# Optimization experiments

Hardware: AMD Instinct MI355X
Metric: run time of the kernel (lower is better)

Reference implementation:

```python
import jax, jax.numpy as jnp
import numpy as np
from math import sqrt

EMBED = 768
HEADS = 12
EPS = 1e-12  # torch F.normalize eps


def setup_inputs() -> dict:
    key = jax.random.key(0)
    ks = jax.random.split(key, 9)
    B, N, E = 8, 4096, EMBED
    s = 1.0 / np.sqrt(E)
    x = jax.random.normal(ks[0], (B, N, E), dtype=jnp.float32)
    Wq = jax.random.normal(ks[1], (E, E), dtype=jnp.float32) * s
    bq = jnp.zeros((E,), dtype=jnp.float32)
    Wk = jax.random.normal(ks[2], (E, E), dtype=jnp.float32) * s
    bk = jnp.zeros((E,), dtype=jnp.float32)
    Wv = jax.random.normal(ks[3], (E, E), dtype=jnp.float32) * s
    bv = jnp.zeros((E,), dtype=jnp.float32)
    Wo = jax.random.normal(ks[4], (E, E), dtype=jnp.float32) * s
    bo = jnp.zeros((E,), dtype=jnp.float32)
    return {"x": x, "Wq": Wq, "bq": bq, "Wk": Wk, "bk": bk,
            "Wv": Wv, "bv": bv, "Wo": Wo, "bo": bo}


def _l2norm_tokens(t):
    # F.normalize(p=2, dim=1): normalize over the token (n) axis
    nrm = jnp.sqrt(jnp.sum(t * t, axis=1, keepdims=True))
    return t / jnp.maximum(nrm, EPS)


def reference(x, Wq, bq, Wk, bk, Wv, bv, Wo, bo):
    B, N, E = x.shape
    h = HEADS
    e = E // h
    q = (x @ Wq + bq).reshape(B, N, h, e)
    k = (x @ Wk + bk).reshape(B, N, h, e)
    v = (x @ Wv + bv).reshape(B, N, h, e)
    q = _l2norm_tokens(q)
    k = _l2norm_tokens(k)
    # cross-covariance attention over channel dim: [b, e, h, e]
    energy = jnp.einsum('bnhe,bnhq->behq', q, k)
    attn = jax.nn.softmax(energy, axis=-1) / sqrt(E)
    out = jnp.einsum('behq,bnhe->bnhq', attn, v)  # [b, n, h, e]
    out = out.reshape(B, N, E)
    return out @ Wo + bo
```

## Files before the change

kernel.cpp:

```cpp
#include <hip/hip_runtime.h>
#include <hip/hip_bf16.h>

typedef short bf16x8 __attribute__((ext_vector_type(8)));
typedef unsigned short u16x8 __attribute__((ext_vector_type(8)));
typedef float f32x4 __attribute__((ext_vector_type(4)));
using bf16 = __hip_bfloat16;

#define EMB 768
#define NHEAD 12
#define BATCH 8
#define NTOK 4096
#define BNTOK 32768

__device__ __forceinline__ float b2f(unsigned short u) {
    union { unsigned int i; float f; } x; x.i = ((unsigned int)u) << 16; return x.f;
}
__device__ __forceinline__ unsigned short f2bu(float f) {
    bf16 h = __float2bfloat16(f);
    return *reinterpret_cast<unsigned short*>(&h);
}

__device__ __forceinline__ void gload_lds16(const void* g, void* l) {
    __builtin_amdgcn_global_load_lds(
        (const __attribute__((address_space(1))) unsigned int*)g,
        (__attribute__((address_space(3))) unsigned int*)l,
        16, 0, 0);
}

__global__ __launch_bounds__(256) void cast_x_kernel(const float* __restrict__ x,
                                                     bf16* __restrict__ xb, int n8) {
    int i = blockIdx.x * blockDim.x + threadIdx.x;
    if (i >= n8) return;
    const float4* xv = (const float4*)x;
    float4 a = xv[i * 2], b = xv[i * 2 + 1];
    u16x8 o;
    o[0] = f2bu(a.x); o[1] = f2bu(a.y); o[2] = f2bu(a.z); o[3] = f2bu(a.w);
    o[4] = f2bu(b.x); o[5] = f2bu(b.y); o[6] = f2bu(b.z); o[7] = f2bu(b.w);
    ((u16x8*)xb)[i] = o;
}

__global__ __launch_bounds__(256) void prep_w_kernel(
    const float* __restrict__ Wq, const float* __restrict__ Wk,
    const float* __restrict__ Wv, const float* __restrict__ Wo,
    const float* __restrict__ bq, const float* __restrict__ bk, const float* __restrict__ bv,
    bf16* __restrict__ WqkvT, bf16* __restrict__ WoT, float* __restrict__ bqkv) {
    const int NQKV = 2304 * 768, NO = 768 * 768;
    int i = blockIdx.x * blockDim.x + threadIdx.x;
    if (i < NQKV) {
        int nrow = i / 768, k = i % 768;
        const float* W = (nrow < 768) ? Wq : (nrow < 1536 ? Wk : Wv);
        int c = nrow % 768;
        WqkvT[i] = __float2bfloat16(W[k * 768 + c]);
    } else if (i < NQKV + NO) {
        int j = i - NQKV; int nrow = j / 768, k = j % 768;
        WoT[j] = __float2bfloat16(Wo[k * 768 + nrow]);
    } else if (i < NQKV + NO + 2304) {
        int j = i - NQKV - NO;
        bqkv[j] = (j < 768) ? bq[j] : (j < 1536 ? bk[j - 768] : bv[j - 1536]);
    }
}

template <int MODE>
__global__ __launch_bounds__(256) void gemm_bt(
    const bf16* __restrict__ A, const bf16* __restrict__ BT,
    int M, int N, int K,
    bf16* __restrict__ Q, bf16* __restrict__ Kb, bf16* __restrict__ V,
    const float* __restrict__ bias,
    float* __restrict__ Cout, const float* __restrict__ bo) {
    __shared__ bf16 As[128 * 32];
    __shared__ bf16 Bs[128 * 32];
    const int tid = threadIdx.x;
    const int lane = tid & 63, wid = tid >> 6;
    const int wm = wid >> 1, wn = wid & 1;
    const int m0 = blockIdx.y * 128, n0 = blockIdx.x * 128;

    f32x4 acc[4][4] = {};
    const int nk = K >> 5;
    const int r0 = tid >> 2, k8 = (tid & 3) << 3;
    const int lrow = lane & 15, lk = lane >> 4;

    for (int kt = 0; kt < nk; ++kt) {
        const bf16* ga0 = A + (size_t)(m0 + r0) * K + kt * 32 + k8;
        const bf16* gb0 = BT + (size_t)(n0 + r0) * K + kt * 32 + k8;
        char* la0 = (char*)As + (wid * 64) * 16;
        char* la1 = (char*)As + (256 + wid * 64) * 16;
        char* lb0 = (char*)Bs + (wid * 64) * 16;
        char* lb1 = (char*)Bs + (256 + wid * 64) * 16;
        gload_lds16(ga0, la0);
        gload_lds16(ga0 + (size_t)64 * K, la1);
        gload_lds16(gb0, lb0);
        gload_lds16(gb0 + (size_t)64 * K, lb1);
        __syncthreads();
        const bf16x8* Av = (const bf16x8*)As;
        const bf16x8* Bv = (const bf16x8*)Bs;
        bf16x8 a[4], b[4];
#pragma unroll
        for (int i = 0; i < 4; ++i) a[i] = Av[(wm * 64 + i * 16 + lrow) * 4 + lk];
#pragma unroll
        for (int i = 0; i < 4; ++i) b[i] = Bv[(wn * 64 + i * 16 + lrow) * 4 + lk];
#pragma unroll
        for (int mi = 0; mi < 4; ++mi)
#pragma unroll
            for (int ni = 0; ni < 4; ++ni)
                acc[mi][ni] = __builtin_amdgcn_mfma_f32_16x16x32_bf16(a[mi], b[ni], acc[mi][ni], 0, 0, 0);
        __syncthreads();
    }

    const int lq = lane >> 4;
    if (MODE == 0) {
        const int which = n0 / 768;
        bf16* O = (which == 0) ? Q : (which == 1 ? Kb : V);
#pragma unroll
        for (int mi = 0; mi < 4; ++mi)
#pragma unroll
            for (int ni = 0; ni < 4; ++ni) {
                int gcol = n0 + wn * 64 + ni * 16 + lrow;
                int col = gcol - which * 768;
                float bia = bias[gcol];
                size_t rbase = (size_t)(m0 + wm * 64 + mi * 16 + lq * 4);
#pragma unroll
                for (int r = 0; r < 4; ++r)
                    O[(rbase + r) * 768 + col] = __float2bfloat16(acc[mi][ni][r] + bia);
            }
    } else {
#pragma unroll
        for (int mi = 0; mi < 4; ++mi)
#pragma unroll
            for (int ni = 0; ni < 4; ++ni) {
                int col = n0 + wn * 64 + ni * 16 + lrow;
                float bia = bo[col];
                size_t rbase = (size_t)(m0 + wm * 64 + mi * 16 + lq * 4);
#pragma unroll
                for (int r = 0; r < 4; ++r)
                    Cout[(rbase + r) * 768 + col] = acc[mi][ni][r] + bia;
            }
    }
}

__global__ __launch_bounds__(256) void sumsq_kernel(
    const bf16* __restrict__ Qb, const bf16* __restrict__ Kb,
    float* __restrict__ ssq, float* __restrict__ ssk) {
    int rc = blockIdx.x, ct = blockIdx.y, b = blockIdx.z;
    int col = ct * 256 + threadIdx.x;
    size_t base = ((size_t)b * NTOK + rc * 256) * 768 + col;
    float sq = 0.f, sk = 0.f;
    for (int i = 0; i < 256; ++i) {
        float q = b2f(*(const unsigned short*)&Qb[base + (size_t)i * 768]);
        float k = b2f(*(const unsigned short*)&Kb[base + (size_t)i * 768]);
        sq += q * q; sk += k * k;
    }
    atomicAdd(&ssq[b * 768 + col], sq);
    atomicAdd(&ssk[b * 768 + col], sk);
}

__global__ __launch_bounds__(256) void gram_kernel(
    const bf16* __restrict__ Qb, const bf16* __restrict__ Kb, float* __restrict__ G) {
    int bh = blockIdx.x >> 2, ch = blockIdx.x & 3;
    int b = bh / NHEAD, h = bh % NHEAD;
    const int t0 = ch * 1024;
    __shared__ float Qs[32][64];
    __shared__ float Ks[32][64];
    int tid = threadIdx.x;
    int e0 = (tid >> 4) << 2, j0 = (tid & 15) << 2;
    float acc[4][4] = {};
    const size_t base = ((size_t)b * NTOK) * 768 + h * 64;
    int lt = tid >> 3, lc = (tid & 7) << 3;
    for (int it = 0; it < 32; ++it) {
        int tok = t0 + it * 32;
        u16x8 qv = *(const u16x8*)(Qb + base + (size_t)(tok + lt) * 768 + lc);
        u16x8 kv = *(const u16x8*)(Kb + base + (size_t)(tok + lt) * 768 + lc);
        __syncthreads();
#pragma unroll
        for (int j = 0; j < 8; ++j) { Qs[lt][lc + j] = b2f(qv[j]); Ks[lt][lc + j] = b2f(kv[j]); }
        __syncthreads();
#pragma unroll
        for (int t = 0; t < 32; ++t) {
            float4 q4 = *(const float4*)&Qs[t][e0];
            float4 k4 = *(const float4*)&Ks[t][j0];
            float q[4] = {q4.x, q4.y, q4.z, q4.w};
            float k[4] = {k4.x, k4.y, k4.z, k4.w};
#pragma unroll
            for (int ii = 0; ii < 4; ++ii)
#pragma unroll
                for (int jj = 0; jj < 4; ++jj) acc[ii][jj] = fmaf(q[ii], k[jj], acc[ii][jj]);
        }
    }
#pragma unroll
    for (int ii = 0; ii < 4; ++ii)
#pragma unroll
        for (int jj = 0; jj < 4; ++jj)
            atomicAdd(&G[(size_t)bh * 4096 + (e0 + ii) * 64 + (j0 + jj)], acc[ii][jj]);
}

__global__ __launch_bounds__(64) void softmax_kernel(
    const float* __restrict__ G, const float* __restrict__ ssq, const float* __restrict__ ssk,
    bf16* __restrict__ attnT) {
    int bh = blockIdx.x; int b = bh / NHEAD, h = bh % NHEAD;
    int e = threadIdx.x;
    const float* g = G + (size_t)bh * 4096 + e * 64;
    float nq = fmaxf(sqrtf(ssq[b * 768 + h * 64 + e]), 1e-12f);
    float row[64];
    float mx = -1e30f;
#pragma unroll
    for (int j = 0; j < 64; ++j) {
        float nk = fmaxf(sqrtf(ssk[b * 768 + h * 64 + j]), 1e-12f);
        float en = g[j] / (nq * nk);
        row[j] = en;
        mx = fmaxf(mx, en);
    }
    float s = 0.f;
#pragma unroll
    for (int j = 0; j < 64; ++j) { row[j] = __expf(row[j] - mx); s += row[j]; }
    float inv = 0.036084391824351615f / s;
#pragma unroll
    for (int j = 0; j < 64; ++j)
        attnT[(size_t)bh * 4096 + j * 64 + e] = __float2bfloat16(row[j] * inv);
}

__global__ __launch_bounds__(256) void pv_kernel(
    const bf16* __restrict__ V, const bf16* __restrict__ attnT, bf16* __restrict__ Y) {
    int tch = blockIdx.x;
    int h = blockIdx.y, b = blockIdx.z;
    int bh = b * NHEAD + h;
    __shared__ bf16 Ats[64 * 64];
    int tid = threadIdx.x, lane = tid & 63, wid = tid >> 6;
    {
        const u16x8* src = (const u16x8*)(attnT + (size_t)bh * 4096);
        u16x8* dst = (u16x8*)Ats;
        dst[tid] = src[tid];
        dst[tid + 256] = src[tid + 256];
    }
    __syncthreads();
    f32x4 acc[4][4] = {};
    const int lrow = lane & 15, lk = lane >> 4;
    const int trow0 = tch * 256 + wid * 64;
#pragma unroll
    for (int ks = 0; ks < 2; ++ks) {
        bf16x8 a[4], bfr[4];
#pragma unroll
        for (int mi = 0; mi < 4; ++mi)
            a[mi] = *(const bf16x8*)(V + (size_t)(b * NTOK + trow0 + mi * 16 + lrow) * 768 +
                                     h * 64 + ks * 32 + lk * 8);
        const bf16x8* Bv = (const bf16x8*)Ats;
#pragma unroll
        for (int ni = 0; ni < 4; ++ni) bfr[ni] = Bv[(ni * 16 + lrow) * 8 + ks * 4 + lk];
#pragma unroll
        for (int mi = 0; mi < 4; ++mi)
#pragma unroll
            for (int ni = 0; ni < 4; ++ni)
                acc[mi][ni] = __builtin_amdgcn_mfma_f32_16x16x32_bf16(a[mi], bfr[ni], acc[mi][ni], 0, 0, 0);
    }
    const int lq = lane >> 4;
#pragma unroll
    for (int mi = 0; mi < 4; ++mi)
#pragma unroll
        for (int ni = 0; ni < 4; ++ni) {
            int col = ni * 16 + lrow;
#pragma unroll
            for (int r = 0; r < 4; ++r) {
                int row = trow0 + mi * 16 + lq * 4 + r;
                Y[(size_t)(b * NTOK + row) * 768 + h * 64 + col] = __float2bfloat16(acc[mi][ni][r]);
            }
        }
}

extern "C" void kernel_launch(void* const* d_in, const int* in_sizes, int n_in,
                              void* d_out, int out_size, void* d_ws, size_t ws_size,
                              hipStream_t stream) {
    const float* x  = (const float*)d_in[0];
    const float* Wq = (const float*)d_in[1];
    const float* bq = (const float*)d_in[2];
    const float* Wk = (const float*)d_in[3];
    const float* bk = (const float*)d_in[4];
    const float* Wv = (const float*)d_in[5];
    const float* bv = (const float*)d_in[6];
    const float* Wo = (const float*)d_in[7];
    const float* bo = (const float*)d_in[8];
    float* out = (float*)d_out;

    char* ws = (char*)d_ws;
    bf16*  xb    = (bf16*)(ws + 0);
    bf16*  WqkvT = (bf16*)(ws + 50331648);
    bf16*  WoT   = (bf16*)(ws + 53870592);
    float* bqkv  = (float*)(ws + 55050240);
    bf16*  Qb    = (bf16*)(ws + 55059456);
    bf16*  Kb    = (bf16*)(ws + 105391104);
    bf16*  Vb    = (bf16*)(ws + 155722752);
    float* ssq   = (float*)(ws + 206054400);
    float* ssk   = (float*)(ws + 206078976);
    float* G     = (float*)(ws + 206103552);
    bf16*  attnT = (bf16*)(ws + 207676416);
    bf16*  Yb    = xb;

    hipMemsetAsync(ws + 206054400, 0, 24576 + 24576 + 1572864, stream);

    cast_x_kernel<<<12288, 256, 0, stream>>>(x, xb, BNTOK * EMB / 8);
    prep_w_kernel<<<9225, 256, 0, stream>>>(Wq, Wk, Wv, Wo, bq, bk, bv, WqkvT, WoT, bqkv);

    gemm_bt<0><<<dim3(18, 256), 256, 0, stream>>>(xb, WqkvT, BNTOK, 2304, 768,
                                                  Qb, Kb, Vb, bqkv, nullptr, nullptr);

    sumsq_kernel<<<dim3(16, 3, 8), 256, 0, stream>>>(Qb, Kb, ssq, ssk);
    gram_kernel<<<384, 256, 0, stream>>>(Qb, Kb, G);
    softmax_kernel<<<96, 64, 0, stream>>>(G, ssq, ssk, attnT);
    pv_kernel<<<dim3(16, NHEAD, BATCH), 256, 0, stream>>>(Vb, attnT, Yb);

    gemm_bt<1><<<dim3(6, 256), 256, 0, stream>>>(Yb, WoT, BNTOK, 768, 768,
                                                 nullptr, nullptr, nullptr, nullptr, out, bo);
}
```

Before: 394.6 us.

## Replace GEMM with 256x256-tile double-buffered pipelined kernel with swizzled LDS

Both projection GEMMs move from a 128x128 single-buffered tile loop to a 256x256 tile with 512 threads, K-step 64, and double-buffered async global-to-LDS loads. Loads for the next stage are issued while MFMAs run on the current one, with vmcnt waits and barriers in place of a full sync each step. The kernel also adds an XOR swizzle on LDS rows/slots to avoid bank conflicts, a workgroup ID remap for L2 locality, and s_setprio around the MFMA blocks. The cost is 128KB of LDS and high register use per block, which limits occupancy, and K is hardcoded to 768.

```diff
diff --git a/kernel.cpp b/kernel.cpp
--- a/kernel.cpp
+++ b/kernel.cpp
@@ -61,78 +61,113 @@
 }
 
 template <int MODE>
-__global__ __launch_bounds__(256) void gemm_bt(
+__global__ __launch_bounds__(512, 2) void gemm256(
     const bf16* __restrict__ A, const bf16* __restrict__ BT,
-    int M, int N, int K,
     bf16* __restrict__ Q, bf16* __restrict__ Kb, bf16* __restrict__ V,
     const float* __restrict__ bias,
     float* __restrict__ Cout, const float* __restrict__ bo) {
-    __shared__ bf16 As[128 * 32];
-    __shared__ bf16 Bs[128 * 32];
+    __shared__ char lds[131072];
+    const int NKT = 12;
     const int tid = threadIdx.x;
     const int lane = tid & 63, wid = tid >> 6;
-    const int wm = wid >> 1, wn = wid & 1;
-    const int m0 = blockIdx.y * 128, n0 = blockIdx.x * 128;
-
-    f32x4 acc[4][4] = {};
-    const int nk = K >> 5;
-    const int r0 = tid >> 2, k8 = (tid & 3) << 3;
+    const int wm = wid >> 2, wn = wid & 3;
     const int lrow = lane & 15, lk = lane >> 4;
-
-    for (int kt = 0; kt < nk; ++kt) {
-        const bf16* ga0 = A + (size_t)(m0 + r0) * K + kt * 32 + k8;
-        const bf16* gb0 = BT + (size_t)(n0 + r0) * K + kt * 32 + k8;
-        char* la0 = (char*)As + (wid * 64) * 16;
-        char* la1 = (char*)As + (256 + wid * 64) * 16;
-        char* lb0 = (char*)Bs + (wid * 64) * 16;
-        char* lb1 = (char*)Bs + (256 + wid * 64) * 16;
-        gload_lds16(ga0, la0);
-        gload_lds16(ga0 + (size_t)64 * K, la1);
-        gload_lds16(gb0, lb0);
-        gload_lds16(gb0 + (size_t)64 * K, lb1);
-        __syncthreads();
-        const bf16x8* Av = (const bf16x8*)As;
-        const bf16x8* Bv = (const bf16x8*)Bs;
-        bf16x8 a[4], b[4];
-#pragma unroll
-        for (int i = 0; i < 4; ++i) a[i] = Av[(wm * 64 + i * 16 + lrow) * 4 + lk];
-#pragma unroll
-        for (int i = 0; i < 4; ++i) b[i] = Bv[(wn * 64 + i * 16 + lrow) * 4 + lk];
-#pragma unroll
-        for (int mi = 0; mi < 4; ++mi)
-#pragma unroll
-            for (int ni = 0; ni < 4; ++ni)
-                acc[mi][ni] = __builtin_amdgcn_mfma_f32_16x16x32_bf16(a[mi], b[ni], acc[mi][ni], 0, 0, 0);
-        __syncthreads();
-    }
-
-    const int lq = lane >> 4;
+    const int xsl = lrow & 3;
+    const int lrsw = lrow ^ ((lrow >> 2) & 1);
+    const int slotb = (lk ^ xsl) << 4;
+
+    int nwg = gridDim.x * gridDim.y;
+    int bid = blockIdx.y * gridDim.x + blockIdx.x;
+    int swz = (bid & 7) * (nwg >> 3) + (bid >> 3);
+    int bx = swz % gridDim.x, by = swz / gridDim.x;
+    const int m0 = by * 256, n0 = bx * 256;
+
+    const int rstg = tid >> 2;
+    const int rl = rstg ^ ((rstg >> 2) & 1);
+    const int sl8 = (((tid & 3) ^ (rl & 3)) << 3);
+
+    f32x4 acc[8][4] = {};
+
+#define STAGE(tbuf, isb, skh, sktv) do {                                          \
+    int skt_ = (sktv); if (skt_ >= NKT) skt_ = NKT - 1;                           \
+    const bf16* gp_ = ((isb) ? BT + (size_t)(n0 + rl) * 768                       \
+                             : A  + (size_t)(m0 + rl) * 768)                      \
+                      + skt_ * 64 + (skh) * 32 + sl8;                             \
+    char* lp_ = lds + (tbuf) * 65536 + (isb) * 32768 + (skh) * 16384 + wid * 1024;\
+    gload_lds16(gp_, lp_);                                                        \
+    gload_lds16(gp_ + (size_t)128 * 768, lp_ + 8192);                             \
+} while (0)
+
+#define COMPUTE(cbuf, KH, CM) do {                                                \
+    const char* ab_ = lds + (cbuf) * 65536 + (KH) * 16384;                        \
+    const char* bb_ = ab_ + 32768;                                                \
+    bf16x8 af_[4], bfv_[4];                                                       \
+    _Pragma("unroll") for (int mi = 0; mi < 4; ++mi) {                            \
+        int pr_ = wm * 128 + (CM) * 64 + mi * 16 + lrsw;                          \
+        af_[mi] = *(const bf16x8*)(ab_ + pr_ * 64 + slotb); }                     \
+    _Pragma("unroll") for (int ni = 0; ni < 4; ++ni) {                            \
+        int pr_ = wn * 64 + ni * 16 + lrsw;                                       \
+        bfv_[ni] = *(const bf16x8*)(bb_ + pr_ * 64 + slotb); }                    \
+    __builtin_amdgcn_s_setprio(1);                                                \
+    _Pragma("unroll") for (int mi = 0; mi < 4; ++mi)                              \
+    _Pragma("unroll") for (int ni = 0; ni < 4; ++ni)                              \
+        acc[(CM) * 4 + mi][ni] = __builtin_amdgcn_mfma_f32_16x16x32_bf16(         \
+            af_[mi], bfv_[ni], acc[(CM) * 4 + mi][ni], 0, 0, 0);                  \
+    __builtin_amdgcn_s_setprio(0);                                                \
+} while (0)
+
+#define VMC8 asm volatile("s_waitcnt vmcnt(8)" ::: "memory")
+#define BAR  __builtin_amdgcn_s_barrier()
+
+    STAGE(0, 0, 0, 0);
+    STAGE(0, 1, 0, 0);
+    STAGE(0, 0, 1, 0);
+    STAGE(0, 1, 1, 0);
+    STAGE(1, 0, 0, 1);
+    STAGE(1, 1, 0, 1);
+    VMC8; BAR;
+
+    for (int i = 0; i < NKT; ++i) {
+        const int cb = i & 1, nb = cb ^ 1;
+        STAGE(nb, 0, 1, i + 1); COMPUTE(cb, 0, 0); BAR;
+        STAGE(nb, 1, 1, i + 1); COMPUTE(cb, 0, 1); VMC8; BAR;
+        STAGE(cb, 0, 0, i + 2); COMPUTE(cb, 1, 0); BAR;
+        STAGE(cb, 1, 0, i + 2); COMPUTE(cb, 1, 1); VMC8; BAR;
+    }
+
+#undef STAGE
+#undef COMPUTE
+#undef VMC8
+#undef BAR
+
+    const int lq = lk;
     if (MODE == 0) {
         const int which = n0 / 768;
         bf16* O = (which == 0) ? Q : (which == 1 ? Kb : V);
-#pragma unroll
-        for (int mi = 0; mi < 4; ++mi)
+        const int cbase = n0 - which * 768 + wn * 64;
+#pragma unroll
+        for (int ri = 0; ri < 8; ++ri)
 #pragma unroll
             for (int ni = 0; ni < 4; ++ni) {
                 int gcol = n0 + wn * 64 + ni * 16 + lrow;
-                int col = gcol - which * 768;
                 float bia = bias[gcol];
-                size_t rbase = (size_t)(m0 + wm * 64 + mi * 16 + lq * 4);
+                int col = cbase + ni * 16 + lrow;
+                size_t r0 = (size_t)(m0 + wm * 128 + ri * 16 + lq * 4);
 #pragma unroll
                 for (int r = 0; r < 4; ++r)
-                    O[(rbase + r) * 768 + col] = __float2bfloat16(acc[mi][ni][r] + bia);
+                    O[(r0 + r) * 768 + col] = __float2bfloat16(acc[ri][ni][r] + bia);
             }
     } else {
 #pragma unroll
-        for (int mi = 0; mi < 4; ++mi)
+        for (int ri = 0; ri < 8; ++ri)
 #pragma unroll
             for (int ni = 0; ni < 4; ++ni) {
                 int col = n0 + wn * 64 + ni * 16 + lrow;
                 float bia = bo[col];
-                size_t rbase = (size_t)(m0 + wm * 64 + mi * 16 + lq * 4);
+                size_t r0 = (size_t)(m0 + wm * 128 + ri * 16 + lq * 4);
 #pragma unroll
                 for (int r = 0; r < 4; ++r)
-                    Cout[(rbase + r) * 768 + col] = acc[mi][ni][r] + bia;
+                    Cout[(r0 + r) * 768 + col] = acc[ri][ni][r] + bia;
             }
     }
 }
@@ -297,14 +332,12 @@
     cast_x_kernel<<<12288, 256, 0, stream>>>(x, xb, BNTOK * EMB / 8);
     prep_w_kernel<<<9225, 256, 0, stream>>>(Wq, Wk, Wv, Wo, bq, bk, bv, WqkvT, WoT, bqkv);
 
-    gemm_bt<0><<<dim3(18, 256), 256, 0, stream>>>(xb, WqkvT, BNTOK, 2304, 768,
-                                                  Qb, Kb, Vb, bqkv, nullptr, nullptr);
+    gemm256<0><<<dim3(9, 128), 512, 0, stream>>>(xb, WqkvT, Qb, Kb, Vb, bqkv, nullptr, nullptr);
 
     sumsq_kernel<<<dim3(16, 3, 8), 256, 0, stream>>>(Qb, Kb, ssq, ssk);
     gram_kernel<<<384, 256, 0, stream>>>(Qb, Kb, G);
     softmax_kernel<<<96, 64, 0, stream>>>(G, ssq, ssk, attnT);
     pv_kernel<<<dim3(16, NHEAD, BATCH), 256, 0, stream>>>(Vb, attnT, Yb);
 
-    gemm_bt<1><<<dim3(6, 256), 256, 0, stream>>>(Yb, WoT, BNTOK, 768, 768,
-                                                 nullptr, nullptr, nullptr, nullptr, out, bo);
-}
+    gemm256<1><<<dim3(3, 128), 512, 0, stream>>>(Yb, WoT, nullptr, nullptr, nullptr, nullptr, out, bo);
+}
```

Measured after the change: 377.0 us. 4.4% less time.
